# Kernel tuning notes

Hardware: AMD Instinct MI355X
Metric: run time of the kernel (lower is better)

Reference implementation:

```python
import jax, jax.numpy as jnp
import numpy as np

B, IN_CH, OUT_CH, STYLE_DIM, K, H, W = 16, 512, 512, 512, 3, 32, 32


def setup_inputs() -> dict:
    key = jax.random.key(0)
    k1, k2, k3, k4 = jax.random.split(key, 4)
    return {
        "x": jax.random.normal(k1, (B, IN_CH, H, W), dtype=jnp.float32),
        "style": jax.random.normal(k2, (B, STYLE_DIM), dtype=jnp.float32),
        "aff_weight": jax.random.normal(k3, (IN_CH, STYLE_DIM), dtype=jnp.float32),
        "aff_bias": jnp.zeros((IN_CH,), dtype=jnp.float32),
        "conv_weight": jax.random.normal(k4, (OUT_CH, IN_CH, K, K), dtype=jnp.float32),
    }


def reference(x, style, aff_weight, aff_bias, conv_weight):
    # EqualizedLinearAct with act='linear': y = style @ (W*scale)^T + bias
    style_dim = aff_weight.shape[1]
    aff_scale = 1.0 / np.sqrt(style_dim)  # gain=1.0
    s = style @ (aff_weight * aff_scale).T + aff_bias + 1.0  # [B, in]

    out_ch, in_ch, k, _ = conv_weight.shape
    w_scale = 1.0 / np.sqrt(in_ch * k * k)  # gain / sqrt(in*k*k)
    # per-sample modulated weights: [B, out, in, k, k]
    w = conv_weight[None, :, :, :, :] * s[:, None, :, None, None] * w_scale
    # demodulation
    d = jax.lax.rsqrt(jnp.sum(w * w, axis=(2, 3, 4), keepdims=True) + 1e-8)
    w = w * d

    # groups=B grouped conv == per-sample conv; up=1, flip_weight=True ->
    # plain cross-correlation (same as torch F.conv2d / lax conv default).
    def conv1(xi, wi):
        # xi: [in, H, W], wi: [out, in, k, k]
        return jax.lax.conv_general_dilated(
            xi[None], wi, window_strides=(1, 1), padding="SAME",
            dimension_numbers=("NCHW", "OIHW", "NCHW"))[0]

    return jax.vmap(conv1)(x, w)  # [B, out, H, W]
```

## Files before the change

kernel.cpp:

```cpp
#include <hip/hip_runtime.h>


#define BATCH   16
#define CIN     512
#define COUT    512
#define IMG     32
#define PAD_IMG 34

static constexpr float AFF_SCALE = 0.044194173824159216f;
static constexpr float W_SCALE   = 0.014731391274719739f;

typedef __bf16 bf16x8 __attribute__((ext_vector_type(8)));
typedef float  f32x4  __attribute__((ext_vector_type(4)));

__device__ inline unsigned short f2bf(float f) {
    union { float f; unsigned int u; } v; v.f = f;
    unsigned int u = v.u;
    unsigned int r = (u + 0x7FFFu + ((u >> 16) & 1u)) >> 16;
    return (unsigned short)r;
}

__device__ inline float waveReduceSum(float v) {
    #pragma unroll
    for (int off = 32; off > 0; off >>= 1) v += __shfl_xor(v, off, 64);
    return v;
}

__global__ void compute_s(const float* __restrict__ style,
                          const float* __restrict__ aw,
                          const float* __restrict__ ab,
                          float* __restrict__ s_out) {
    const int i = blockIdx.x * 4 + (threadIdx.x >> 6);
    const int b = blockIdx.y;
    const int lane = threadIdx.x & 63;
    float sum = 0.f;
    #pragma unroll
    for (int k = 0; k < 512; k += 64)
        sum += style[b * 512 + k + lane] * aw[i * 512 + k + lane];
    sum = waveReduceSum(sum);
    if (lane == 0) s_out[b * 512 + i] = sum * AFF_SCALE + ab[i] + 1.0f;
}

__global__ void repack_w(const float* __restrict__ cw,
                         unsigned short* __restrict__ w_t,
                         float* __restrict__ wsq) {
    const int idx = blockIdx.x * 256 + threadIdx.x;
    const float* src = cw + (size_t)idx * 9;
    float acc = 0.f;
    #pragma unroll
    for (int e = 0; e < 9; ++e) {
        float v = src[e];
        acc += v * v;
        w_t[e * (COUT * CIN) + idx] = f2bf(v);
    }
    wsq[idx] = acc;
}

__global__ void compute_scale(const float* __restrict__ s_in,
                              const float* __restrict__ wsq,
                              float* __restrict__ scl) {
    const int o = blockIdx.x * 4 + (threadIdx.x >> 6);
    const int b = blockIdx.y;
    const int lane = threadIdx.x & 63;
    float sum = 0.f;
    #pragma unroll
    for (int i = 0; i < 512; i += 64) {
        float sv = s_in[b * 512 + i + lane];
        sum += sv * sv * wsq[o * 512 + i + lane];
    }
    sum = waveReduceSum(sum);
    if (lane == 0)
        scl[b * 512 + o] = W_SCALE * rsqrtf(W_SCALE * W_SCALE * sum + 1e-8f);
}

__global__ void build_xpad(const float* __restrict__ x,
                           const float* __restrict__ s_in,
                           unsigned short* __restrict__ xpad) {
    const int c0 = blockIdx.x * 64;
    const int hh = blockIdx.y;
    const int b  = blockIdx.z;
    const int tid = threadIdx.x;
    unsigned short* rowbase = xpad + (((size_t)b * PAD_IMG + hh) * PAD_IMG) * 512;

    if (hh == 0 || hh == PAD_IMG - 1) {
        for (int j = tid; j < 34 * 32; j += 256) {
            int ww = j >> 5, cp = (j & 31) * 2;
            *(unsigned int*)(rowbase + (size_t)ww * 512 + c0 + cp) = 0u;
        }
        return;
    }

    __shared__ float t[64][33];
    const int h = hh - 1;
    {
        const int wx = tid & 31;
        const int cb = (tid >> 5) * 8;
        const float* xb = x + (((size_t)b * 512 + c0 + cb) * IMG + h) * IMG + wx;
        #pragma unroll
        for (int j = 0; j < 8; ++j)
            t[cb + j][wx] = xb[(size_t)j * (IMG * IMG)] * s_in[b * 512 + c0 + cb + j];
    }
    __syncthreads();
    {
        const int p  = tid >> 3;
        const int cc = (tid & 7) * 8;
        unsigned short* dst = rowbase + (size_t)(p + 1) * 512 + c0 + cc;
        uint4 pk;
        pk.x = (unsigned)f2bf(t[cc + 0][p]) | ((unsigned)f2bf(t[cc + 1][p]) << 16);
        pk.y = (unsigned)f2bf(t[cc + 2][p]) | ((unsigned)f2bf(t[cc + 3][p]) << 16);
        pk.z = (unsigned)f2bf(t[cc + 4][p]) | ((unsigned)f2bf(t[cc + 5][p]) << 16);
        pk.w = (unsigned)f2bf(t[cc + 6][p]) | ((unsigned)f2bf(t[cc + 7][p]) << 16);
        *(uint4*)dst = pk;
    }
    if (tid < 64) {
        int ww = (tid >> 5) ? (PAD_IMG - 1) : 0;
        int cp = (tid & 31) * 2;
        *(unsigned int*)(rowbase + (size_t)ww * 512 + c0 + cp) = 0u;
    }
}

__global__ __launch_bounds__(256, 2) void conv_mfma(
    const unsigned short* __restrict__ wt,
    const unsigned short* __restrict__ xpad,
    const float* __restrict__ scl,
    float* __restrict__ out)
{
    __shared__ unsigned short Alds[128 * 32];
    __shared__ unsigned short Blds[128 * 32];
    __shared__ float sclds[128];

    const int tid = threadIdx.x;
    const int b   = blockIdx.z;
    const int m0  = blockIdx.x * 128;
    const int h0  = blockIdx.y * 4;

    if (tid < 128) sclds[tid] = scl[b * 512 + m0 + tid];

    const int wid  = tid >> 6;
    const int lane = tid & 63;
    const int wm = wid & 1, wn = wid >> 1;

    const f32x4 vzero = {0.f, 0.f, 0.f, 0.f};
    f32x4 acc[4][4];
    #pragma unroll
    for (int i = 0; i < 4; ++i)
        #pragma unroll
        for (int j = 0; j < 4; ++j) acc[i][j] = vzero;

    int aOff[2], bOff[2], ldsBase[2];
    #pragma unroll
    for (int r = 0; r < 2; ++r) {
        int f   = r * 256 + tid;
        int row = f >> 2;
        int col = (f & 3) * 8;
        aOff[r] = row * 512 + col;
        bOff[r] = ((row >> 5) * PAD_IMG + (row & 31)) * 512 + col;
        ldsBase[r] = (r * 256 + wid * 64) * 8;
    }

    const int arow = (wm * 64 + (lane & 15)) * 32 + (lane >> 4) * 8;
    const int brow = (wn * 64 + (lane & 15)) * 32 + (lane >> 4) * 8;

    for (int e = 0; e < 9; ++e) {
        const int kh = e / 3, kw = e % 3;
        const unsigned short* Abase = wt + (size_t)e * (COUT * CIN) + (size_t)m0 * 512;
        const unsigned short* Bbase =
            xpad + (((size_t)b * PAD_IMG + h0 + kh) * PAD_IMG + kw) * 512;
        for (int kc = 0; kc < 512; kc += 32) {
            __syncthreads();
            #pragma unroll
            for (int r = 0; r < 2; ++r)
                __builtin_amdgcn_global_load_lds(
                    (const __attribute__((address_space(1))) void*)(Abase + aOff[r] + kc),
                    (__attribute__((address_space(3))) void*)(&Alds[ldsBase[r]]),
                    16, 0, 0);
            #pragma unroll
            for (int r = 0; r < 2; ++r)
                __builtin_amdgcn_global_load_lds(
                    (const __attribute__((address_space(1))) void*)(Bbase + bOff[r] + kc),
                    (__attribute__((address_space(3))) void*)(&Blds[ldsBase[r]]),
                    16, 0, 0);
            __syncthreads();

            bf16x8 af[4], bfr[4];
            #pragma unroll
            for (int mi = 0; mi < 4; ++mi)
                af[mi] = *(const bf16x8*)(&Alds[arow + mi * 16 * 32]);
            #pragma unroll
            for (int ni = 0; ni < 4; ++ni)
                bfr[ni] = *(const bf16x8*)(&Blds[brow + ni * 16 * 32]);
            #pragma unroll
            for (int mi = 0; mi < 4; ++mi)
                #pragma unroll
                for (int ni = 0; ni < 4; ++ni)
                    acc[mi][ni] = __builtin_amdgcn_mfma_f32_16x16x32_bf16(
                        af[mi], bfr[ni], acc[mi][ni], 0, 0, 0);
        }
    }

    const int colp = lane & 15;
    const int rowq = (lane >> 4) * 4;
    const int p0 = h0 * 32;
    #pragma unroll
    for (int mi = 0; mi < 4; ++mi) {
        #pragma unroll
        for (int ni = 0; ni < 4; ++ni) {
            const int p = p0 + wn * 64 + ni * 16 + colp;
            #pragma unroll
            for (int r2 = 0; r2 < 4; ++r2) {
                const int ol = wm * 64 + mi * 16 + rowq + r2;
                out[(((size_t)b * 512 + m0 + ol) << 10) + p] =
                    acc[mi][ni][r2] * sclds[ol];
            }
        }
    }
}

extern "C" void kernel_launch(void* const* d_in, const int* in_sizes, int n_in,
                              void* d_out, int out_size, void* d_ws, size_t ws_size,
                              hipStream_t stream) {
    const float* x     = (const float*)d_in[0];
    const float* style = (const float*)d_in[1];
    const float* aw    = (const float*)d_in[2];
    const float* ab    = (const float*)d_in[3];
    const float* cw    = (const float*)d_in[4];
    float* out = (float*)d_out;

    char* ws = (char*)d_ws;
    float* s_buf          = (float*)(ws);
    float* scl            = (float*)(ws + 32768);
    float* wsq            = (float*)(ws + 65536);
    unsigned short* w_t   = (unsigned short*)(ws + 1114112);
    unsigned short* x_pad = (unsigned short*)(ws + 5832704);

    compute_s<<<dim3(128, 16), 256, 0, stream>>>(style, aw, ab, s_buf);
    repack_w<<<dim3(1024), 256, 0, stream>>>(cw, w_t, wsq);
    compute_scale<<<dim3(128, 16), 256, 0, stream>>>(s_buf, wsq, scl);
    build_xpad<<<dim3(8, 34, 16), 256, 0, stream>>>(x, s_buf, x_pad);
    conv_mfma<<<dim3(4, 8, 16), 256, 0, stream>>>(w_t, x_pad, scl, out);
}
```

Measured before the change: 203.1 us.

## Fuse prep kernels, stage weight repack via LDS, remap conv blocks per XCD

```diff
diff --git a/kernel.cpp b/kernel.cpp
--- a/kernel.cpp
+++ b/kernel.cpp
@@ -26,34 +26,42 @@
     return v;
 }
 
-__global__ void compute_s(const float* __restrict__ style,
-                          const float* __restrict__ aw,
-                          const float* __restrict__ ab,
-                          float* __restrict__ s_out) {
-    const int i = blockIdx.x * 4 + (threadIdx.x >> 6);
-    const int b = blockIdx.y;
-    const int lane = threadIdx.x & 63;
-    float sum = 0.f;
-    #pragma unroll
-    for (int k = 0; k < 512; k += 64)
-        sum += style[b * 512 + k + lane] * aw[i * 512 + k + lane];
-    sum = waveReduceSum(sum);
-    if (lane == 0) s_out[b * 512 + i] = sum * AFF_SCALE + ab[i] + 1.0f;
-}
-
-__global__ void repack_w(const float* __restrict__ cw,
-                         unsigned short* __restrict__ w_t,
-                         float* __restrict__ wsq) {
-    const int idx = blockIdx.x * 256 + threadIdx.x;
-    const float* src = cw + (size_t)idx * 9;
-    float acc = 0.f;
-    #pragma unroll
-    for (int e = 0; e < 9; ++e) {
-        float v = src[e];
-        acc += v * v;
-        w_t[e * (COUT * CIN) + idx] = f2bf(v);
-    }
-    wsq[idx] = acc;
+__global__ void prep1(const float* __restrict__ cw,
+                      const float* __restrict__ style,
+                      const float* __restrict__ aw,
+                      const float* __restrict__ ab,
+                      unsigned short* __restrict__ w_t,
+                      float* __restrict__ wsq,
+                      float* __restrict__ s_out) {
+    const int tid = threadIdx.x;
+    if (blockIdx.x < 1024) {
+        __shared__ float wl[2304];
+        const float* src = cw + (size_t)blockIdx.x * 2304;
+        for (int j = tid; j < 2304; j += 256) wl[j] = src[j];
+        __syncthreads();
+        const int idx = blockIdx.x * 256 + tid;
+        const int base = tid * 9;
+        float acc = 0.f;
+        #pragma unroll
+        for (int e = 0; e < 9; ++e) {
+            float v = wl[base + e];
+            acc += v * v;
+            w_t[e * (COUT * CIN) + idx] = f2bf(v);
+        }
+        wsq[idx] = acc;
+    } else {
+        const int q = blockIdx.x - 1024;
+        const int b = q >> 7;
+        const int i = (q & 127) * 4 + (tid >> 6);
+        const int lane = tid & 63;
+        float sum = 0.f;
+        #pragma unroll
+        for (int k = 0; k < 512; k += 64)
+            sum += style[b * 512 + k + lane] * aw[i * 512 + k + lane];
+        sum = waveReduceSum(sum);
+        if (lane == 0)
+            s_out[b * 512 + i] = sum * AFF_SCALE + ab[i] + 1.0f;
+    }
 }
 
 __global__ void compute_scale(const float* __restrict__ s_in,
@@ -130,9 +138,13 @@
     __shared__ float sclds[128];
 
     const int tid = threadIdx.x;
-    const int b   = blockIdx.z;
-    const int m0  = blockIdx.x * 128;
-    const int h0  = blockIdx.y * 4;
+    const int id    = blockIdx.x;
+    const int xcd   = id & 7;
+    const int local = id >> 3;
+    const int gp    = xcd * 16 + (local >> 2);
+    const int m0  = (local & 3) * 128;
+    const int h0  = (gp & 7) * 4;
+    const int b   = gp >> 3;
 
     if (tid < 128) sclds[tid] = scl[b * 512 + m0 + tid];
 
@@ -233,9 +245,8 @@
     unsigned short* w_t   = (unsigned short*)(ws + 1114112);
     unsigned short* x_pad = (unsigned short*)(ws + 5832704);
 
-    compute_s<<<dim3(128, 16), 256, 0, stream>>>(style, aw, ab, s_buf);
-    repack_w<<<dim3(1024), 256, 0, stream>>>(cw, w_t, wsq);
+    prep1<<<dim3(3072), 256, 0, stream>>>(cw, style, aw, ab, w_t, wsq, s_buf);
     compute_scale<<<dim3(128, 16), 256, 0, stream>>>(s_buf, wsq, scl);
     build_xpad<<<dim3(8, 34, 16), 256, 0, stream>>>(x, s_buf, x_pad);
-    conv_mfma<<<dim3(4, 8, 16), 256, 0, stream>>>(w_t, x_pad, scl, out);
-}
+    conv_mfma<<<dim3(512), 256, 0, stream>>>(w_t, x_pad, scl, out);
+}
```

Result: faster. 193.3 us (-4.8%).
